# Performance work log

Hardware: AMD Instinct MI355X
Metric: run time of the kernel (lower is better)

The kernel has to match this reference:

```python
import jax, jax.numpy as jnp
import numpy as np

EPS = 1e-5  # BatchNorm eps
B, T, D, H, C = 64, 1024, 128, 1024, 128


def _glorot(k, shape):
    lim = float(np.sqrt(6.0 / (shape[0] + shape[1])))
    return jax.random.uniform(k, shape, minval=-lim, maxval=lim, dtype=jnp.float32)


def _bn(x, g, b, m, v):
    # eval-mode BatchNorm1d over the channel (last) dim
    return (x - m) * (g * jax.lax.rsqrt(v + EPS)) + b


def _cell(x, h, c, Wih, Whh, bias):
    # PyTorch LSTM gate order: i, f, g, o
    z = x @ Wih.T + h @ Whh.T + bias
    i, f, g, o = jnp.split(z, 4, axis=-1)
    c = jax.nn.sigmoid(f) * c + jax.nn.sigmoid(i) * jnp.tanh(g)
    h = jax.nn.sigmoid(o) * jnp.tanh(c)
    return h, c


def setup_inputs() -> dict:
    key = jax.random.key(0)
    ks = jax.random.split(key, 24)
    d = {}
    d['x'] = jax.random.normal(ks[0], (B, T, D), dtype=jnp.float32)
    # input BN (eval mode running stats + affine)
    d['ibn_g'] = jnp.ones((D,), jnp.float32); d['ibn_b'] = jnp.zeros((D,), jnp.float32)
    d['ibn_m'] = 0.1 * jax.random.normal(ks[1], (D,), jnp.float32)
    d['ibn_v'] = jnp.ones((D,), jnp.float32)
    # encoder LSTM (2 layers)
    d['enc_Wih0'] = _glorot(ks[2], (4 * H, D)); d['enc_Whh0'] = _glorot(ks[3], (4 * H, H))
    d['enc_b0'] = jnp.zeros((4 * H,), jnp.float32)
    d['enc_Wih1'] = _glorot(ks[4], (4 * H, H)); d['enc_Whh1'] = _glorot(ks[5], (4 * H, H))
    d['enc_b1'] = jnp.zeros((4 * H,), jnp.float32)
    # decoder LSTM (2 layers), layer0 input = num_classes
    d['dec_Wih0'] = _glorot(ks[6], (4 * H, C)); d['dec_Whh0'] = _glorot(ks[7], (4 * H, H))
    d['dec_b0'] = jnp.zeros((4 * H,), jnp.float32)
    d['dec_Wih1'] = _glorot(ks[8], (4 * H, H)); d['dec_Whh1'] = _glorot(ks[9], (4 * H, H))
    d['dec_b1'] = jnp.zeros((4 * H,), jnp.float32)
    # hidden BN
    d['hbn_g'] = jnp.ones((H,), jnp.float32); d['hbn_b'] = jnp.zeros((H,), jnp.float32)
    d['hbn_m'] = 0.1 * jax.random.normal(ks[10], (H,), jnp.float32)
    d['hbn_v'] = jnp.ones((H,), jnp.float32)
    # fc head: Linear(H,H) -> BN -> ReLU -> (Dropout=identity in eval) -> Linear(H,C)
    d['fc1_W'] = _glorot(ks[11], (H, H)); d['fc1_b'] = jnp.zeros((H,), jnp.float32)
    d['fbn_g'] = jnp.ones((H,), jnp.float32); d['fbn_b'] = jnp.zeros((H,), jnp.float32)
    d['fbn_m'] = 0.1 * jax.random.normal(ks[12], (H,), jnp.float32)
    d['fbn_v'] = jnp.ones((H,), jnp.float32)
    d['fc2_W'] = _glorot(ks[13], (C, H)); d['fc2_b'] = jnp.zeros((C,), jnp.float32)
    return d


def reference(x, ibn_g, ibn_b, ibn_m, ibn_v,
              enc_Wih0, enc_Whh0, enc_b0, enc_Wih1, enc_Whh1, enc_b1,
              dec_Wih0, dec_Whh0, dec_b0, dec_Wih1, dec_Whh1, dec_b1,
              hbn_g, hbn_b, hbn_m, hbn_v,
              fc1_W, fc1_b, fbn_g, fbn_b, fbn_m, fbn_v, fc2_W, fc2_b):
    b, t, _ = x.shape
    h = enc_Whh0.shape[1]
    c_dim = fc2_W.shape[0]
    xn = _bn(x, ibn_g, ibn_b, ibn_m, ibn_v)  # (B,T,D), per-channel BN

    def enc_step(carry, xt):
        h0, c0, h1, c1 = carry
        h0, c0 = _cell(xt, h0, c0, enc_Wih0, enc_Whh0, enc_b0)
        h1, c1 = _cell(h0, h1, c1, enc_Wih1, enc_Whh1, enc_b1)
        return (h0, c0, h1, c1), None

    z = jnp.zeros((b, h), x.dtype)
    (h0, c0, h1, c1), _ = jax.lax.scan(enc_step, (z, z, z, z), jnp.swapaxes(xn, 0, 1))

    def dec_step(carry, _):
        d0, e0, d1, e1, y = carry
        d0, e0 = _cell(y, d0, e0, dec_Wih0, dec_Whh0, dec_b0)
        d1, e1 = _cell(d0, d1, e1, dec_Wih1, dec_Whh1, dec_b1)
        hb = _bn(d1, hbn_g, hbn_b, hbn_m, hbn_v)
        f1 = jax.nn.relu(_bn(hb @ fc1_W.T + fc1_b, fbn_g, fbn_b, fbn_m, fbn_v))
        pred = f1 @ fc2_W.T + fc2_b  # (B, C)
        return (d0, e0, d1, e1, pred), pred

    y0 = jnp.zeros((b, c_dim), x.dtype)
    _, preds = jax.lax.scan(dec_step, (h0, c0, h1, c1, y0), None, length=t)
    return jnp.swapaxes(preds, 0, 1)  # (B, T, C)
```

## Files before the change

### kernel.cpp

```cpp
#include <hip/hip_runtime.h>
#include <hip/hip_bf16.h>


typedef __hip_bfloat16 hbf16;
typedef __bf16 bf16x8 __attribute__((ext_vector_type(8)));
typedef float f32x4 __attribute__((ext_vector_type(4)));
#define DEVI static __device__ __forceinline__

#define PITCH 2056
#define PITCH0 1160

DEVI float sigf(float x) { return 1.0f / (1.0f + __expf(-x)); }

DEVI bf16x8 as_bf(f32x4 v) { union { f32x4 f; bf16x8 b; } u; u.f = v; return u.b; }

DEVI void st_u32_coh(void* p, unsigned int v) {
  __hip_atomic_store((unsigned int*)p, v, __ATOMIC_RELAXED, __HIP_MEMORY_SCOPE_AGENT);
}
DEVI void st_u64_coh(void* p, unsigned long long v) {
  __hip_atomic_store((unsigned long long*)p, v, __ATOMIC_RELAXED, __HIP_MEMORY_SCOPE_AGENT);
}
DEVI void st_f32_coh(float* p, float v) {
  __hip_atomic_store(p, v, __ATOMIC_RELAXED, __HIP_MEMORY_SCOPE_AGENT);
}
DEVI unsigned short bf_bits(float v) {
  union { __hip_bfloat16 b; unsigned short s; } u;
  u.b = __float2bfloat16(v);
  return u.s;
}

DEVI void ld32_wait(f32x4* b, const hbf16* ap) {
  asm volatile(
    "global_load_dwordx4 %0, %32, off sc0 sc1\n\t"
    "global_load_dwordx4 %1, %32, off offset:64 sc0 sc1\n\t"
    "global_load_dwordx4 %2, %32, off offset:128 sc0 sc1\n\t"
    "global_load_dwordx4 %3, %32, off offset:192 sc0 sc1\n\t"
    "global_load_dwordx4 %4, %32, off offset:256 sc0 sc1\n\t"
    "global_load_dwordx4 %5, %32, off offset:320 sc0 sc1\n\t"
    "global_load_dwordx4 %6, %32, off offset:384 sc0 sc1\n\t"
    "global_load_dwordx4 %7, %32, off offset:448 sc0 sc1\n\t"
    "global_load_dwordx4 %8, %32, off offset:512 sc0 sc1\n\t"
    "global_load_dwordx4 %9, %32, off offset:576 sc0 sc1\n\t"
    "global_load_dwordx4 %10, %32, off offset:640 sc0 sc1\n\t"
    "global_load_dwordx4 %11, %32, off offset:704 sc0 sc1\n\t"
    "global_load_dwordx4 %12, %32, off offset:768 sc0 sc1\n\t"
    "global_load_dwordx4 %13, %32, off offset:832 sc0 sc1\n\t"
    "global_load_dwordx4 %14, %32, off offset:896 sc0 sc1\n\t"
    "global_load_dwordx4 %15, %32, off offset:960 sc0 sc1\n\t"
    "global_load_dwordx4 %16, %32, off offset:1024 sc0 sc1\n\t"
    "global_load_dwordx4 %17, %32, off offset:1088 sc0 sc1\n\t"
    "global_load_dwordx4 %18, %32, off offset:1152 sc0 sc1\n\t"
    "global_load_dwordx4 %19, %32, off offset:1216 sc0 sc1\n\t"
    "global_load_dwordx4 %20, %32, off offset:1280 sc0 sc1\n\t"
    "global_load_dwordx4 %21, %32, off offset:1344 sc0 sc1\n\t"
    "global_load_dwordx4 %22, %32, off offset:1408 sc0 sc1\n\t"
    "global_load_dwordx4 %23, %32, off offset:1472 sc0 sc1\n\t"
    "global_load_dwordx4 %24, %32, off offset:1536 sc0 sc1\n\t"
    "global_load_dwordx4 %25, %32, off offset:1600 sc0 sc1\n\t"
    "global_load_dwordx4 %26, %32, off offset:1664 sc0 sc1\n\t"
    "global_load_dwordx4 %27, %32, off offset:1728 sc0 sc1\n\t"
    "global_load_dwordx4 %28, %32, off offset:1792 sc0 sc1\n\t"
    "global_load_dwordx4 %29, %32, off offset:1856 sc0 sc1\n\t"
    "global_load_dwordx4 %30, %32, off offset:1920 sc0 sc1\n\t"
    "global_load_dwordx4 %31, %32, off offset:1984 sc0 sc1\n\t"
    "s_waitcnt vmcnt(0)"
    : "=&v"(b[0]), "=&v"(b[1]), "=&v"(b[2]), "=&v"(b[3]),
      "=&v"(b[4]), "=&v"(b[5]), "=&v"(b[6]), "=&v"(b[7]),
      "=&v"(b[8]), "=&v"(b[9]), "=&v"(b[10]), "=&v"(b[11]),
      "=&v"(b[12]), "=&v"(b[13]), "=&v"(b[14]), "=&v"(b[15]),
      "=&v"(b[16]), "=&v"(b[17]), "=&v"(b[18]), "=&v"(b[19]),
      "=&v"(b[20]), "=&v"(b[21]), "=&v"(b[22]), "=&v"(b[23]),
      "=&v"(b[24]), "=&v"(b[25]), "=&v"(b[26]), "=&v"(b[27]),
      "=&v"(b[28]), "=&v"(b[29]), "=&v"(b[30]), "=&v"(b[31])
    : "v"(ap) : "memory");
}

DEVI void ld4x8_wait(f32x4* b, const hbf16* a0, const hbf16* a1,
                     const hbf16* a2, const hbf16* a3) {
  asm volatile(
    "global_load_dwordx4 %0, %32, off sc0 sc1\n\t"
    "global_load_dwordx4 %1, %32, off offset:64 sc0 sc1\n\t"
    "global_load_dwordx4 %2, %32, off offset:128 sc0 sc1\n\t"
    "global_load_dwordx4 %3, %32, off offset:192 sc0 sc1\n\t"
    "global_load_dwordx4 %4, %32, off offset:256 sc0 sc1\n\t"
    "global_load_dwordx4 %5, %32, off offset:320 sc0 sc1\n\t"
    "global_load_dwordx4 %6, %32, off offset:384 sc0 sc1\n\t"
    "global_load_dwordx4 %7, %32, off offset:448 sc0 sc1\n\t"
    "global_load_dwordx4 %8, %33, off sc0 sc1\n\t"
    "global_load_dwordx4 %9, %33, off offset:64 sc0 sc1\n\t"
    "global_load_dwordx4 %10, %33, off offset:128 sc0 sc1\n\t"
    "global_load_dwordx4 %11, %33, off offset:192 sc0 sc1\n\t"
    "global_load_dwordx4 %12, %33, off offset:256 sc0 sc1\n\t"
    "global_load_dwordx4 %13, %33, off offset:320 sc0 sc1\n\t"
    "global_load_dwordx4 %14, %33, off offset:384 sc0 sc1\n\t"
    "global_load_dwordx4 %15, %33, off offset:448 sc0 sc1\n\t"
    "global_load_dwordx4 %16, %34, off sc0 sc1\n\t"
    "global_load_dwordx4 %17, %34, off offset:64 sc0 sc1\n\t"
    "global_load_dwordx4 %18, %34, off offset:128 sc0 sc1\n\t"
    "global_load_dwordx4 %19, %34, off offset:192 sc0 sc1\n\t"
    "global_load_dwordx4 %20, %34, off offset:256 sc0 sc1\n\t"
    "global_load_dwordx4 %21, %34, off offset:320 sc0 sc1\n\t"
    "global_load_dwordx4 %22, %34, off offset:384 sc0 sc1\n\t"
    "global_load_dwordx4 %23, %34, off offset:448 sc0 sc1\n\t"
    "global_load_dwordx4 %24, %35, off sc0 sc1\n\t"
    "global_load_dwordx4 %25, %35, off offset:64 sc0 sc1\n\t"
    "global_load_dwordx4 %26, %35, off offset:128 sc0 sc1\n\t"
    "global_load_dwordx4 %27, %35, off offset:192 sc0 sc1\n\t"
    "global_load_dwordx4 %28, %35, off offset:256 sc0 sc1\n\t"
    "global_load_dwordx4 %29, %35, off offset:320 sc0 sc1\n\t"
    "global_load_dwordx4 %30, %35, off offset:384 sc0 sc1\n\t"
    "global_load_dwordx4 %31, %35, off offset:448 sc0 sc1\n\t"
    "s_waitcnt vmcnt(0)"
    : "=&v"(b[0]), "=&v"(b[1]), "=&v"(b[2]), "=&v"(b[3]),
      "=&v"(b[4]), "=&v"(b[5]), "=&v"(b[6]), "=&v"(b[7]),
      "=&v"(b[8]), "=&v"(b[9]), "=&v"(b[10]), "=&v"(b[11]),
      "=&v"(b[12]), "=&v"(b[13]), "=&v"(b[14]), "=&v"(b[15]),
      "=&v"(b[16]), "=&v"(b[17]), "=&v"(b[18]), "=&v"(b[19]),
      "=&v"(b[20]), "=&v"(b[21]), "=&v"(b[22]), "=&v"(b[23]),
      "=&v"(b[24]), "=&v"(b[25]), "=&v"(b[26]), "=&v"(b[27]),
      "=&v"(b[28]), "=&v"(b[29]), "=&v"(b[30]), "=&v"(b[31])
    : "v"(a0), "v"(a1), "v"(a2), "v"(a3) : "memory");
}

DEVI void gbar(int* cnt8, int e) {
  asm volatile("s_waitcnt vmcnt(0) lgkmcnt(0)" ::: "memory");
  __syncthreads();
  if (threadIdx.x == 0)
    __hip_atomic_fetch_add(&cnt8[(blockIdx.x & 7) * 16], 1,
                           __ATOMIC_RELAXED, __HIP_MEMORY_SCOPE_AGENT);
  if (threadIdx.x < 8) {
    while (__hip_atomic_load(&cnt8[threadIdx.x * 16], __ATOMIC_RELAXED,
                             __HIP_MEMORY_SCOPE_AGENT) < e * 32)
      __builtin_amdgcn_s_sleep(1);
  }
  __syncthreads();
}

DEVI void fill_w(hbf16* W, int pitch, int koff, const hbf16* __restrict__ Wg,
                 int Kg, int base_h) {
  for (int r = (int)(threadIdx.x >> 3); r < 32; r += 32) {
    int g = r >> 3, hc = r & 7;
    const hbf16* src = Wg + (long)(g * 1024 + base_h + hc) * Kg;
    hbf16* dst = W + r * pitch + koff;
    for (int k = (threadIdx.x & 7) * 8; k < Kg; k += 64)
      *reinterpret_cast<bf16x8*>(dst + k) =
          *reinterpret_cast<const bf16x8*>(src + k);
  }
}

DEVI void seg_asm(f32x4& a0, f32x4& a1, const hbf16* __restrict__ A, long lda,
                  const hbf16* W, int pitch, int koff, int w, int q, int r16) {
  const hbf16* ap = A + (long)(w * 16 + r16) * lda + q * 8;
  const hbf16* w0 = W + r16 * pitch + koff + q * 8;
  const hbf16* w1 = W + (16 + r16) * pitch + koff + q * 8;
  f32x4 b[32];
  ld32_wait(b, ap);
#pragma unroll
  for (int k = 0; k < 32; ++k) {
    bf16x8 av = as_bf(b[k]);
    bf16x8 b0 = *reinterpret_cast<const bf16x8*>(w0 + k * 32);
    bf16x8 b1 = *reinterpret_cast<const bf16x8*>(w1 + k * 32);
    a0 = __builtin_amdgcn_mfma_f32_16x16x32_bf16(av, b0, a0, 0, 0, 0);
    a1 = __builtin_amdgcn_mfma_f32_16x16x32_bf16(av, b1, a1, 0, 0, 0);
  }
}

DEVI void seg_x(f32x4& a0, f32x4& a1, const hbf16* __restrict__ A, long lda,
                const hbf16* W, int pitch, int w, int q, int r16) {
  const hbf16* ap = A + (long)(w * 16 + r16) * lda + q * 8;
  const hbf16* w0 = W + r16 * pitch + q * 8;
  const hbf16* w1 = W + (16 + r16) * pitch + q * 8;
#pragma unroll
  for (int k = 0; k < 128; k += 32) {
    bf16x8 av = *reinterpret_cast<const bf16x8*>(ap + k);
    bf16x8 b0 = *reinterpret_cast<const bf16x8*>(w0 + k);
    bf16x8 b1 = *reinterpret_cast<const bf16x8*>(w1 + k);
    a0 = __builtin_amdgcn_mfma_f32_16x16x32_bf16(av, b0, a0, 0, 0, 0);
    a1 = __builtin_amdgcn_mfma_f32_16x16x32_bf16(av, b1, a1, 0, 0, 0);
  }
}

DEVI void mm4_asm(f32x4* pa, const hbf16* __restrict__ abase, const bf16x8* fr) {
  f32x4 b[32];
  ld4x8_wait(b, abase, abase + 16384, abase + 32768, abase + 49152);
#pragma unroll
  for (int i = 0; i < 8; ++i)
#pragma unroll
    for (int mt = 0; mt < 4; ++mt)
      pa[mt] = __builtin_amdgcn_mfma_f32_16x16x32_bf16(
          as_bf(b[mt * 8 + i]), fr[i], pa[mt], 0, 0, 0);
}

DEVI void cell(f32x4 a0, f32x4 a1, float bb0, float bb1, float* cst,
               hbf16* __restrict__ hout, int base_h, int lane, int w) {
  int q = lane >> 4, c = lane & 15;
#pragma unroll
  for (int r = 0; r < 4; ++r) {
    float z0 = a0[r] + bb0;
    float z1 = a1[r] + bb1;
    float zf = __shfl(z0, lane | 8, 64);
    float zo = __shfl(z1, lane | 8, 64);
    float hv = 0.f;
    if (c < 8) {
      float cn = sigf(zf) * cst[r] + sigf(z0) * tanhf(z1);
      cst[r] = cn;
      hv = sigf(zo) * tanhf(cn);
    }
    unsigned short my = bf_bits(hv);
    unsigned short nb = (unsigned short)__shfl((int)my, lane ^ 1, 64);
    if (c < 8 && (c & 1) == 0) {
      unsigned int pk = (unsigned int)my | ((unsigned int)nb << 16);
      st_u32_coh(hout + (long)(w * 16 + q * 4 + r) * 1024 + base_h + c, pk);
    }
  }
}

DEVI void store_c(const float* cst, float* cbuf, int hcol_g, int lane, int w) {
  int q = lane >> 4, c = lane & 15;
  if (c < 8) {
#pragma unroll
    for (int r = 0; r < 4; ++r)
      st_f32_coh(&cbuf[(long)(w * 16 + q * 4 + r) * 1024 + hcol_g], cst[r]);
  }
}

__global__ __launch_bounds__(256, 1) void k_enc(
    const hbf16* __restrict__ xb,
    const hbf16* __restrict__ Wih0f, const hbf16* __restrict__ Whh0,
    const hbf16* __restrict__ Wih1, const hbf16* __restrict__ Whh1,
    const float* __restrict__ b0f, const float* __restrict__ b1f,
    hbf16* h0_0, hbf16* h0_1, hbf16* h1_0, hbf16* h1_1,
    float* c0buf, float* c1buf, int* flags) {
  __shared__ hbf16 W[32 * PITCH];
  int wg = blockIdx.x, tid = threadIdx.x;
  int lane = tid & 63, w = tid >> 6, q = lane >> 4, c = lane & 15;
  bool isL0 = wg < 128;
  int cu = isL0 ? wg : wg - 128;
  int base_h = cu * 8;
  if (isL0) {
    fill_w(W, PITCH0, 0, Wih0f, 128, base_h);
    fill_w(W, PITCH0, 128, Whh0, 1024, base_h);
  } else {
    fill_w(W, PITCH, 0, Wih1, 1024, base_h);
    fill_w(W, PITCH, 1024, Whh1, 1024, base_h);
  }
  __syncthreads();
  const float* bias = isL0 ? b0f : b1f;
  float bb0 = bias[(c >> 3) * 1024 + base_h + (c & 7)];
  float bb1 = bias[(2 + (c >> 3)) * 1024 + base_h + (c & 7)];
  float cst[4] = {0.f, 0.f, 0.f, 0.f};
  int hcol_g = base_h + (c & 7);

  for (int t = 0; t <= 1024; ++t) {
    if (isL0) {
      if (t < 1024) {
        f32x4 a0 = {0.f,0.f,0.f,0.f}, a1 = {0.f,0.f,0.f,0.f};
        const hbf16* h0r = (t & 1) ? h0_0 : h0_1;
        seg_asm(a0, a1, h0r, 1024L, W, PITCH0, 128, w, q, c);
        seg_x(a0, a1, xb + (long)t * 128, 131072L, W, PITCH0, w, q, c);
        hbf16* h0w = (t & 1) ? h0_1 : h0_0;
        cell(a0, a1, bb0, bb1, cst, h0w, base_h, lane, w);
        if (t == 1023) store_c(cst, c0buf, hcol_g, lane, w);
      }
    } else {
      if (t >= 1) {
        f32x4 a0 = {0.f,0.f,0.f,0.f}, a1 = {0.f,0.f,0.f,0.f};
        const hbf16* h0r = (t & 1) ? h0_0 : h0_1;
        seg_asm(a0, a1, h0r, 1024L, W, PITCH, 0, w, q, c);
        const hbf16* h1r = (t & 1) ? h1_1 : h1_0;
        seg_asm(a0, a1, h1r, 1024L, W, PITCH, 1024, w, q, c);
        hbf16* h1w = (t & 1) ? h1_0 : h1_1;
        cell(a0, a1, bb0, bb1, cst, h1w, base_h, lane, w);
        if (t == 1024) store_c(cst, c1buf, hcol_g, lane, w);
      }
    }
    if (t < 1024) gbar(flags, t + 1);
  }
}

__global__ __launch_bounds__(256, 1) void k_dec(
    const hbf16* __restrict__ Wfold, const hbf16* __restrict__ Whh0d,
    const hbf16* __restrict__ Wih1d, const hbf16* __restrict__ Whh1d,
    const float* __restrict__ b0t, const float* __restrict__ b0p,
    const float* __restrict__ b1d,
    const hbf16* __restrict__ fc1Wf, const float* __restrict__ fc1bf,
    const float* __restrict__ fs2, const float* __restrict__ fadd2,
    const hbf16* __restrict__ fc2Wb, const float* __restrict__ fc2b,
    hbf16* d0_0, hbf16* d0_1, hbf16* d1_0, hbf16* d1_1, hbf16* f1b,
    const float* __restrict__ c0buf, const float* __restrict__ c1buf,
    float* __restrict__ out, int* flags) {
  __shared__ hbf16 W[32 * PITCH];
  __shared__ float bounce[4][64][16];
  int wg = blockIdx.x, tid = threadIdx.x;
  int lane = tid & 63, w = tid >> 6, q = lane >> 4, c = lane & 15;
  bool isP1 = wg < 128;
  int cu = isP1 ? wg : wg - 128;
  int base_h = cu * 8;
  if (isP1) {
    fill_w(W, PITCH, 0, Wfold, 1024, base_h);
    fill_w(W, PITCH, 1024, Whh0d, 1024, base_h);
  } else {
    fill_w(W, PITCH, 0, Wih1d, 1024, base_h);
    fill_w(W, PITCH, 1024, Whh1d, 1024, base_h);
  }
  __syncthreads();
  int gi0 = (c >> 3) * 1024 + base_h + (c & 7);
  int gi1 = (2 + (c >> 3)) * 1024 + base_h + (c & 7);
  float bt0, bt1, bp0, bp1;
  if (isP1) { bt0 = b0t[gi0]; bt1 = b0t[gi1]; bp0 = b0p[gi0]; bp1 = b0p[gi1]; }
  else      { bt0 = b1d[gi0]; bt1 = b1d[gi1]; bp0 = bt0;      bp1 = bt1; }
  int hcol_g = base_h + (c & 7);
  float cst[4] = {0.f, 0.f, 0.f, 0.f};
  {
    const float* cb = isP1 ? c0buf : c1buf;
    if (c < 8) {
#pragma unroll
      for (int r = 0; r < 4; ++r)
        cst[r] = cb[(long)(w * 16 + q * 4 + r) * 1024 + hcol_g];
    }
  }
  bool isP3 = (wg < 64);
  bool isPred = (wg >= 128 && wg < 136);
  bf16x8 fr[8];
#pragma unroll
  for (int i = 0; i < 8; ++i) fr[i] = bf16x8{0,0,0,0,0,0,0,0};
  float e_b[4] = {0,0,0,0}, e_s[4] = {0,0,0,0}, e_a[4] = {0,0,0,0};
  int red_row = tid >> 2, red_c4 = (tid & 3) * 4;
  if (isP3) {
    const hbf16* fp = fc1Wf + (long)(wg * 16 + c) * 1024 + w * 256 + q * 8;
#pragma unroll
    for (int i = 0; i < 8; ++i) fr[i] = *reinterpret_cast<const bf16x8*>(fp + i * 32);
#pragma unroll
    for (int i = 0; i < 4; ++i) {
      int col = wg * 16 + red_c4 + i;
      e_b[i] = fc1bf[col]; e_s[i] = fs2[col]; e_a[i] = fadd2[col];
    }
  } else if (isPred) {
    const hbf16* fp = fc2Wb + (long)((wg - 128) * 16 + c) * 1024 + w * 256 + q * 8;
#pragma unroll
    for (int i = 0; i < 8; ++i) fr[i] = *reinterpret_cast<const bf16x8*>(fp + i * 32);
#pragma unroll
    for (int i = 0; i < 4; ++i) e_b[i] = fc2b[(wg - 128) * 16 + red_c4 + i];
  }

  f32x4 r0 = {0.f,0.f,0.f,0.f}, r1 = {0.f,0.f,0.f,0.f};

  for (int t = 0; t <= 1024; ++t) {
    if (isP1 && t < 1024) {
      f32x4 a0 = r0, a1 = r1;
      if (t > 0) {
        seg_asm(a0, a1, f1b, 1024L, W, PITCH, 0, w, q, c);
      } else {
        seg_asm(a0, a1, d0_1, 1024L, W, PITCH, 1024, w, q, c);
      }
      float B0 = (t > 0) ? bt0 : bp0, B1 = (t > 0) ? bt1 : bp1;
      hbf16* d0w = (t & 1) ? d0_1 : d0_0;
      cell(a0, a1, B0, B1, cst, d0w, base_h, lane, w);
    }
    if (!isP1 && t == 0) {
      seg_asm(r0, r1, d1_1, 1024L, W, PITCH, 1024, w, q, c);
    }
    if (isPred && t >= 1) {
      f32x4 pa[4] = {{0.f,0.f,0.f,0.f},{0.f,0.f,0.f,0.f},{0.f,0.f,0.f,0.f},{0.f,0.f,0.f,0.f}};
      mm4_asm(pa, f1b + (long)c * 1024 + w * 256 + q * 8, fr);
#pragma unroll
      for (int mt = 0; mt < 4; ++mt)
#pragma unroll
        for (int r = 0; r < 4; ++r) bounce[w][mt * 16 + q * 4 + r][c] = pa[mt][r];
      __syncthreads();
#pragma unroll
      for (int i = 0; i < 4; ++i) {
        int cc = red_c4 + i;
        float s = bounce[0][red_row][cc] + bounce[1][red_row][cc] +
                  bounce[2][red_row][cc] + bounce[3][red_row][cc] + e_b[i];
        out[(long)red_row * 131072 + (long)(t - 1) * 128 + (wg - 128) * 16 + cc] = s;
      }
    }
    if (t == 1024) break;
    gbar(flags, 3 * t + 1);
    if (!isP1) {
      f32x4 a0 = r0, a1 = r1;
      const hbf16* d0c = (t & 1) ? d0_1 : d0_0;
      seg_asm(a0, a1, d0c, 1024L, W, PITCH, 0, w, q, c);
      hbf16* d1w = (t & 1) ? d1_1 : d1_0;
      cell(a0, a1, bt0, bt1, cst, d1w, base_h, lane, w);
    } else if (isP3 && t < 1023) {
      r0 = f32x4{0.f,0.f,0.f,0.f}; r1 = f32x4{0.f,0.f,0.f,0.f};
      const hbf16* d0n = (t & 1) ? d0_1 : d0_0;
      seg_asm(r0, r1, d0n, 1024L, W, PITCH, 1024, w, q, c);
    }
    gbar(flags, 3 * t + 2);
    if (isP3) {
      const hbf16* d1c = (t & 1) ? d1_1 : d1_0;
      f32x4 pa[4] = {{0.f,0.f,0.f,0.f},{0.f,0.f,0.f,0.f},{0.f,0.f,0.f,0.f},{0.f,0.f,0.f,0.f}};
      mm4_asm(pa, d1c + (long)c * 1024 + w * 256 + q * 8, fr);
#pragma unroll
      for (int mt = 0; mt < 4; ++mt)
#pragma unroll
        for (int r = 0; r < 4; ++r) bounce[w][mt * 16 + q * 4 + r][c] = pa[mt][r];
      __syncthreads();
#pragma unroll
      for (int i = 0; i < 4; ++i) {
        int cc = red_c4 + i;
        float s = bounce[0][red_row][cc] + bounce[1][red_row][cc] +
                  bounce[2][red_row][cc] + bounce[3][red_row][cc];
        float v = fmaxf((s + e_b[i]) * e_s[i] + e_a[i], 0.f);
        bounce[0][red_row][cc] = v;
      }
      {
        union { unsigned short s4[4]; unsigned long long u; } pk;
#pragma unroll
        for (int i = 0; i < 4; ++i) pk.s4[i] = bf_bits(bounce[0][red_row][red_c4 + i]);
        st_u64_coh(f1b + (long)red_row * 1024 + wg * 16 + red_c4, pk.u);
      }
    } else if (isP1 && t < 1023) {
      r0 = f32x4{0.f,0.f,0.f,0.f}; r1 = f32x4{0.f,0.f,0.f,0.f};
      const hbf16* d0n = (t & 1) ? d0_1 : d0_0;
      seg_asm(r0, r1, d0n, 1024L, W, PITCH, 1024, w, q, c);
    }
    if (!isP1 && t < 1023) {
      r0 = f32x4{0.f,0.f,0.f,0.f}; r1 = f32x4{0.f,0.f,0.f,0.f};
      const hbf16* d1n = (t & 1) ? d1_1 : d1_0;
      seg_asm(r0, r1, d1n, 1024L, W, PITCH, 1024, w, q, c);
    }
    gbar(flags, 3 * t + 3);
  }
}


__global__ void k_cast_bf16(const float* __restrict__ s, hbf16* __restrict__ d, long n) {
  long i = (long)blockIdx.x * blockDim.x + threadIdx.x;
  long stride = (long)gridDim.x * blockDim.x;
  for (; i < n; i += stride) d[i] = __float2bfloat16(s[i]);
}

__global__ void k_prep_b0tot(const float* __restrict__ dec_b0, const float* __restrict__ dWih0,
                             const float* __restrict__ fc2b, float* __restrict__ b0d_tot) {
  int n = blockIdx.x * 256 + threadIdx.x;
  float acc = 0.f;
  for (int cc = 0; cc < 128; ++cc) acc += dWih0[n * 128 + cc] * fc2b[cc];
  b0d_tot[n] = dec_b0[n] + acc;
}

__global__ void k_fold_ih0(const float* __restrict__ g, const float* __restrict__ bb,
                           const float* __restrict__ m, const float* __restrict__ v,
                           const float* __restrict__ Wm, const float* __restrict__ b0,
                           hbf16* __restrict__ Wf, float* __restrict__ biasf) {
  int n = blockIdx.x * 256 + threadIdx.x;
  float acc = 0.f;
  for (int k = 0; k < 128; ++k) {
    float s = g[k] * rsqrtf(v[k] + 1e-5f);
    float tt = bb[k] - m[k] * s;
    float wv = Wm[n * 128 + k];
    Wf[n * 128 + k] = __float2bfloat16(wv * s);
    acc += tt * wv;
  }
  biasf[n] = b0[n] + acc;
}

__global__ void k_fold_fc1(const float* __restrict__ hg, const float* __restrict__ hb,
                           const float* __restrict__ hm, const float* __restrict__ hv,
                           const float* __restrict__ Wm, const float* __restrict__ fb,
                           const float* __restrict__ fg, const float* __restrict__ fbb,
                           const float* __restrict__ fm, const float* __restrict__ fv,
                           hbf16* __restrict__ Wf, float* __restrict__ bfo,
                           float* __restrict__ fs2, float* __restrict__ fadd2) {
  int n = blockIdx.x * 256 + threadIdx.x;
  float acc = 0.f;
  for (int k = 0; k < 1024; ++k) {
    float s = hg[k] * rsqrtf(hv[k] + 1e-5f);
    float tt = hb[k] - hm[k] * s;
    float wv = Wm[(long)n * 1024 + k];
    Wf[(long)n * 1024 + k] = __float2bfloat16(wv * s);
    acc += tt * wv;
  }
  bfo[n] = fb[n] + acc;
  float s2 = fg[n] * rsqrtf(fv[n] + 1e-5f);
  fs2[n] = s2;
  fadd2[n] = fbb[n] - fm[n] * s2;
}

__global__ void k_fold_wf(const float* __restrict__ Wih0d, const float* __restrict__ fc2W,
                          hbf16* __restrict__ Wfold) {
  long gid = (long)blockIdx.x * 256 + threadIdx.x;
  int n = (int)(gid >> 10), jcol = (int)(gid & 1023);
  float acc = 0.f;
  for (int cc = 0; cc < 128; ++cc)
    acc += Wih0d[n * 128 + cc] * fc2W[cc * 1024 + jcol];
  Wfold[gid] = __float2bfloat16(acc);
}


extern "C" void kernel_launch(void* const* d_in, const int* in_sizes, int n_in,
                              void* d_out, int out_size, void* d_ws, size_t ws_size,
                              hipStream_t stream) {
  (void)in_sizes; (void)n_in; (void)out_size; (void)ws_size;
  const float* x     = (const float*)d_in[0];
  const float* ibn_g = (const float*)d_in[1];
  const float* ibn_b = (const float*)d_in[2];
  const float* ibn_m = (const float*)d_in[3];
  const float* ibn_v = (const float*)d_in[4];
  const float* eWih0 = (const float*)d_in[5];
  const float* eWhh0 = (const float*)d_in[6];
  const float* e_b0  = (const float*)d_in[7];
  const float* eWih1 = (const float*)d_in[8];
  const float* eWhh1 = (const float*)d_in[9];
  const float* e_b1  = (const float*)d_in[10];
  const float* dWih0 = (const float*)d_in[11];
  const float* dWhh0 = (const float*)d_in[12];
  const float* d_b0  = (const float*)d_in[13];
  const float* dWih1 = (const float*)d_in[14];
  const float* dWhh1 = (const float*)d_in[15];
  const float* d_b1  = (const float*)d_in[16];
  const float* hbn_g = (const float*)d_in[17];
  const float* hbn_b = (const float*)d_in[18];
  const float* hbn_m = (const float*)d_in[19];
  const float* hbn_v = (const float*)d_in[20];
  const float* fc1_W = (const float*)d_in[21];
  const float* fc1_b = (const float*)d_in[22];
  const float* fbn_g = (const float*)d_in[23];
  const float* fbn_b = (const float*)d_in[24];
  const float* fbn_m = (const float*)d_in[25];
  const float* fbn_v = (const float*)d_in[26];
  const float* fc2_W = (const float*)d_in[27];
  const float* fc2_b = (const float*)d_in[28];
  float* out = (float*)d_out;

  char* p = (char*)d_ws;
  auto alloc = [&](size_t bytes) -> void* {
    void* r = (void*)p;
    p += (bytes + 255) & ~(size_t)255;
    return r;
  };
  hbf16* xb     = (hbf16*)alloc(64L * 1024 * 128 * 2);
  hbf16* Wih0f  = (hbf16*)alloc(4096L * 128 * 2);
  hbf16* Whh0e  = (hbf16*)alloc(4096L * 1024 * 2);
  hbf16* Wih1e  = (hbf16*)alloc(4096L * 1024 * 2);
  hbf16* Whh1e  = (hbf16*)alloc(4096L * 1024 * 2);
  hbf16* Wfold  = (hbf16*)alloc(4096L * 1024 * 2);
  hbf16* Whh0d  = (hbf16*)alloc(4096L * 1024 * 2);
  hbf16* Wih1d  = (hbf16*)alloc(4096L * 1024 * 2);
  hbf16* Whh1d  = (hbf16*)alloc(4096L * 1024 * 2);
  hbf16* fc1Wf  = (hbf16*)alloc(1024L * 1024 * 2);
  hbf16* fc2Wb  = (hbf16*)alloc(128L * 1024 * 2);
  float* bias0f = (float*)alloc(4096 * 4);
  float* b0dtot = (float*)alloc(4096 * 4);
  float* fc1bf  = (float*)alloc(1024 * 4);
  float* fs2    = (float*)alloc(1024 * 4);
  float* fadd2  = (float*)alloc(1024 * 4);
  char* st = p;
  hbf16* h0_0 = (hbf16*)alloc(64L * 1024 * 2);
  hbf16* h0_1 = (hbf16*)alloc(64L * 1024 * 2);
  hbf16* h1_0 = (hbf16*)alloc(64L * 1024 * 2);
  hbf16* h1_1 = (hbf16*)alloc(64L * 1024 * 2);
  float* c0b  = (float*)alloc(64L * 1024 * 4);
  float* c1b  = (float*)alloc(64L * 1024 * 4);
  hbf16* f1b  = (hbf16*)alloc(64L * 1024 * 2);
  int*   flagsE = (int*)alloc(256 * 4);
  int*   flagsD = (int*)alloc(256 * 4);
  size_t stbytes = (size_t)(p - st);

  hipMemsetAsync(st, 0, stbytes, stream);

  k_cast_bf16<<<4096, 256, 0, stream>>>(x, xb, 64L * 1024 * 128);
  k_cast_bf16<<<2048, 256, 0, stream>>>(eWhh0, Whh0e, 4096L * 1024);
  k_cast_bf16<<<2048, 256, 0, stream>>>(eWih1, Wih1e, 4096L * 1024);
  k_cast_bf16<<<2048, 256, 0, stream>>>(eWhh1, Whh1e, 4096L * 1024);
  k_cast_bf16<<<2048, 256, 0, stream>>>(dWhh0, Whh0d, 4096L * 1024);
  k_cast_bf16<<<2048, 256, 0, stream>>>(dWih1, Wih1d, 4096L * 1024);
  k_cast_bf16<<<2048, 256, 0, stream>>>(dWhh1, Whh1d, 4096L * 1024);
  k_cast_bf16<<<512, 256, 0, stream>>>(fc2_W, fc2Wb, 128L * 1024);
  k_prep_b0tot<<<16, 256, 0, stream>>>(d_b0, dWih0, fc2_b, b0dtot);
  k_fold_ih0<<<16, 256, 0, stream>>>(ibn_g, ibn_b, ibn_m, ibn_v, eWih0, e_b0, Wih0f, bias0f);
  k_fold_fc1<<<4, 256, 0, stream>>>(hbn_g, hbn_b, hbn_m, hbn_v, fc1_W, fc1_b,
                                    fbn_g, fbn_b, fbn_m, fbn_v, fc1Wf, fc1bf, fs2, fadd2);
  k_fold_wf<<<16384, 256, 0, stream>>>(dWih0, fc2_W, Wfold);

  k_enc<<<256, 256, 0, stream>>>(xb, Wih0f, Whh0e, Wih1e, Whh1e, bias0f, e_b1,
                                 h0_0, h0_1, h1_0, h1_1, c0b, c1b, flagsE);

  k_dec<<<256, 256, 0, stream>>>(Wfold, Whh0d, Wih1d, Whh1d, b0dtot, d_b0, d_b1,
                                 fc1Wf, fc1bf, fs2, fadd2, fc2Wb, fc2_b,
                                 h0_0, h0_1, h1_0, h1_1, f1b, c0b, c1b, out, flagsD);
}
```

Baseline: 39.17 ms.

## Use per-timestep ring buffers for hidden states to allow plain cached loads

Measured after the change: 39.69 ms. About the same (+1.3%).

```diff
diff --git a/kernel.cpp b/kernel.cpp
--- a/kernel.cpp
+++ b/kernel.cpp
@@ -9,6 +9,8 @@
 
 #define PITCH 2056
 #define PITCH0 1160
+#define SLE 66048L
+#define SLDATA 65536L
 
 DEVI float sigf(float x) { return 1.0f / (1.0f + __expf(-x)); }
 
@@ -165,6 +167,21 @@
   }
 }
 
+DEVI void seg_pl(f32x4& a0, f32x4& a1, const hbf16* A,
+                 const hbf16* W, int pitch, int koff, int w, int q, int r16) {
+  const hbf16* ap = A + (long)(w * 16 + r16) * 1024L + q * 8;
+  const hbf16* w0 = W + r16 * pitch + koff + q * 8;
+  const hbf16* w1 = W + (16 + r16) * pitch + koff + q * 8;
+#pragma unroll
+  for (int k = 0; k < 32; ++k) {
+    bf16x8 av = *reinterpret_cast<const bf16x8*>(ap + k * 32);
+    bf16x8 b0 = *reinterpret_cast<const bf16x8*>(w0 + k * 32);
+    bf16x8 b1 = *reinterpret_cast<const bf16x8*>(w1 + k * 32);
+    a0 = __builtin_amdgcn_mfma_f32_16x16x32_bf16(av, b0, a0, 0, 0, 0);
+    a1 = __builtin_amdgcn_mfma_f32_16x16x32_bf16(av, b1, a1, 0, 0, 0);
+  }
+}
+
 DEVI void seg_x(f32x4& a0, f32x4& a1, const hbf16* __restrict__ A, long lda,
                 const hbf16* W, int pitch, int w, int q, int r16) {
   const hbf16* ap = A + (long)(w * 16 + r16) * lda + q * 8;
@@ -191,8 +208,24 @@
           as_bf(b[mt * 8 + i]), fr[i], pa[mt], 0, 0, 0);
 }
 
+DEVI void mm4_pl(f32x4* pa, const hbf16* abase, const bf16x8* fr) {
+  f32x4 b[32];
+#pragma unroll
+  for (int mt = 0; mt < 4; ++mt)
+#pragma unroll
+    for (int i = 0; i < 8; ++i)
+      b[mt * 8 + i] = *reinterpret_cast<const f32x4*>(
+          reinterpret_cast<const char*>(abase + mt * 16384) + i * 64);
+#pragma unroll
+  for (int i = 0; i < 8; ++i)
+#pragma unroll
+    for (int mt = 0; mt < 4; ++mt)
+      pa[mt] = __builtin_amdgcn_mfma_f32_16x16x32_bf16(
+          as_bf(b[mt * 8 + i]), fr[i], pa[mt], 0, 0, 0);
+}
+
 DEVI void cell(f32x4 a0, f32x4 a1, float bb0, float bb1, float* cst,
-               hbf16* __restrict__ hout, int base_h, int lane, int w) {
+               hbf16* hout, int base_h, int lane, int w) {
   int q = lane >> 4, c = lane & 15;
 #pragma unroll
   for (int r = 0; r < 4; ++r) {
@@ -224,12 +257,14 @@
   }
 }
 
+template<int RING>
 __global__ __launch_bounds__(256, 1) void k_enc(
     const hbf16* __restrict__ xb,
     const hbf16* __restrict__ Wih0f, const hbf16* __restrict__ Whh0,
     const hbf16* __restrict__ Wih1, const hbf16* __restrict__ Whh1,
     const float* __restrict__ b0f, const float* __restrict__ b1f,
     hbf16* h0_0, hbf16* h0_1, hbf16* h1_0, hbf16* h1_1,
+    hbf16* rh0, hbf16* rh1,
     float* c0buf, float* c1buf, int* flags) {
   __shared__ hbf16 W[32 * PITCH];
   int wg = blockIdx.x, tid = threadIdx.x;
@@ -255,22 +290,34 @@
     if (isL0) {
       if (t < 1024) {
         f32x4 a0 = {0.f,0.f,0.f,0.f}, a1 = {0.f,0.f,0.f,0.f};
-        const hbf16* h0r = (t & 1) ? h0_0 : h0_1;
-        seg_asm(a0, a1, h0r, 1024L, W, PITCH0, 128, w, q, c);
-        seg_x(a0, a1, xb + (long)t * 128, 131072L, W, PITCH0, w, q, c);
-        hbf16* h0w = (t & 1) ? h0_1 : h0_0;
-        cell(a0, a1, bb0, bb1, cst, h0w, base_h, lane, w);
+        if constexpr (RING) {
+          seg_pl(a0, a1, rh0 + (long)t * SLE, W, PITCH0, 128, w, q, c);
+          seg_x(a0, a1, xb + (long)t * 128, 131072L, W, PITCH0, w, q, c);
+          cell(a0, a1, bb0, bb1, cst, rh0 + (long)(t + 1) * SLE, base_h, lane, w);
+        } else {
+          const hbf16* h0r = (t & 1) ? h0_0 : h0_1;
+          seg_asm(a0, a1, h0r, 1024L, W, PITCH0, 128, w, q, c);
+          seg_x(a0, a1, xb + (long)t * 128, 131072L, W, PITCH0, w, q, c);
+          hbf16* h0w = (t & 1) ? h0_1 : h0_0;
+          cell(a0, a1, bb0, bb1, cst, h0w, base_h, lane, w);
+        }
         if (t == 1023) store_c(cst, c0buf, hcol_g, lane, w);
       }
     } else {
       if (t >= 1) {
         f32x4 a0 = {0.f,0.f,0.f,0.f}, a1 = {0.f,0.f,0.f,0.f};
-        const hbf16* h0r = (t & 1) ? h0_0 : h0_1;
-        seg_asm(a0, a1, h0r, 1024L, W, PITCH, 0, w, q, c);
-        const hbf16* h1r = (t & 1) ? h1_1 : h1_0;
-        seg_asm(a0, a1, h1r, 1024L, W, PITCH, 1024, w, q, c);
-        hbf16* h1w = (t & 1) ? h1_0 : h1_1;
-        cell(a0, a1, bb0, bb1, cst, h1w, base_h, lane, w);
+        if constexpr (RING) {
+          seg_pl(a0, a1, rh0 + (long)t * SLE, W, PITCH, 0, w, q, c);
+          seg_pl(a0, a1, rh1 + (long)(t - 1) * SLE, W, PITCH, 1024, w, q, c);
+          cell(a0, a1, bb0, bb1, cst, rh1 + (long)t * SLE, base_h, lane, w);
+        } else {
+          const hbf16* h0r = (t & 1) ? h0_0 : h0_1;
+          seg_asm(a0, a1, h0r, 1024L, W, PITCH, 0, w, q, c);
+          const hbf16* h1r = (t & 1) ? h1_1 : h1_0;
+          seg_asm(a0, a1, h1r, 1024L, W, PITCH, 1024, w, q, c);
+          hbf16* h1w = (t & 1) ? h1_0 : h1_1;
+          cell(a0, a1, bb0, bb1, cst, h1w, base_h, lane, w);
+        }
         if (t == 1024) store_c(cst, c1buf, hcol_g, lane, w);
       }
     }
@@ -278,6 +325,7 @@
   }
 }
 
+template<int RING>
 __global__ __launch_bounds__(256, 1) void k_dec(
     const hbf16* __restrict__ Wfold, const hbf16* __restrict__ Whh0d,
     const hbf16* __restrict__ Wih1d, const hbf16* __restrict__ Whh1d,
@@ -287,6 +335,8 @@
     const float* __restrict__ fs2, const float* __restrict__ fadd2,
     const hbf16* __restrict__ fc2Wb, const float* __restrict__ fc2b,
     hbf16* d0_0, hbf16* d0_1, hbf16* d1_0, hbf16* d1_1, hbf16* f1b,
+    hbf16* rf1, hbf16* rd0, hbf16* rd1,
+    const hbf16* h0fin, const hbf16* h1fin,
     const float* __restrict__ c0buf, const float* __restrict__ c1buf,
     float* __restrict__ out, int* flags) {
   __shared__ hbf16 W[32 * PITCH];
@@ -349,20 +399,32 @@
     if (isP1 && t < 1024) {
       f32x4 a0 = r0, a1 = r1;
       if (t > 0) {
-        seg_asm(a0, a1, f1b, 1024L, W, PITCH, 0, w, q, c);
+        if constexpr (RING)
+          seg_pl(a0, a1, rf1 + (long)(t - 1) * SLE, W, PITCH, 0, w, q, c);
+        else
+          seg_asm(a0, a1, f1b, 1024L, W, PITCH, 0, w, q, c);
       } else {
-        seg_asm(a0, a1, d0_1, 1024L, W, PITCH, 1024, w, q, c);
+        if constexpr (RING)
+          seg_pl(a0, a1, h0fin, W, PITCH, 1024, w, q, c);
+        else
+          seg_asm(a0, a1, d0_1, 1024L, W, PITCH, 1024, w, q, c);
       }
       float B0 = (t > 0) ? bt0 : bp0, B1 = (t > 0) ? bt1 : bp1;
-      hbf16* d0w = (t & 1) ? d0_1 : d0_0;
+      hbf16* d0w = RING ? (rd0 + (long)t * SLE) : ((t & 1) ? d0_1 : d0_0);
       cell(a0, a1, B0, B1, cst, d0w, base_h, lane, w);
     }
     if (!isP1 && t == 0) {
-      seg_asm(r0, r1, d1_1, 1024L, W, PITCH, 1024, w, q, c);
+      if constexpr (RING)
+        seg_pl(r0, r1, h1fin, W, PITCH, 1024, w, q, c);
+      else
+        seg_asm(r0, r1, d1_1, 1024L, W, PITCH, 1024, w, q, c);
     }
     if (isPred && t >= 1) {
       f32x4 pa[4] = {{0.f,0.f,0.f,0.f},{0.f,0.f,0.f,0.f},{0.f,0.f,0.f,0.f},{0.f,0.f,0.f,0.f}};
-      mm4_asm(pa, f1b + (long)c * 1024 + w * 256 + q * 8, fr);
+      if constexpr (RING)
+        mm4_pl(pa, rf1 + (long)(t - 1) * SLE + (long)c * 1024 + w * 256 + q * 8, fr);
+      else
+        mm4_asm(pa, f1b + (long)c * 1024 + w * 256 + q * 8, fr);
 #pragma unroll
       for (int mt = 0; mt < 4; ++mt)
 #pragma unroll
@@ -380,20 +442,33 @@
     gbar(flags, 3 * t + 1);
     if (!isP1) {
       f32x4 a0 = r0, a1 = r1;
-      const hbf16* d0c = (t & 1) ? d0_1 : d0_0;
-      seg_asm(a0, a1, d0c, 1024L, W, PITCH, 0, w, q, c);
-      hbf16* d1w = (t & 1) ? d1_1 : d1_0;
-      cell(a0, a1, bt0, bt1, cst, d1w, base_h, lane, w);
+      if constexpr (RING) {
+        seg_pl(a0, a1, rd0 + (long)t * SLE, W, PITCH, 0, w, q, c);
+        cell(a0, a1, bt0, bt1, cst, rd1 + (long)t * SLE, base_h, lane, w);
+      } else {
+        const hbf16* d0c = (t & 1) ? d0_1 : d0_0;
+        seg_asm(a0, a1, d0c, 1024L, W, PITCH, 0, w, q, c);
+        hbf16* d1w = (t & 1) ? d1_1 : d1_0;
+        cell(a0, a1, bt0, bt1, cst, d1w, base_h, lane, w);
+      }
     } else if (isP3 && t < 1023) {
       r0 = f32x4{0.f,0.f,0.f,0.f}; r1 = f32x4{0.f,0.f,0.f,0.f};
-      const hbf16* d0n = (t & 1) ? d0_1 : d0_0;
-      seg_asm(r0, r1, d0n, 1024L, W, PITCH, 1024, w, q, c);
+      if constexpr (RING)
+        seg_pl(r0, r1, rd0 + (long)t * SLE, W, PITCH, 1024, w, q, c);
+      else {
+        const hbf16* d0n = (t & 1) ? d0_1 : d0_0;
+        seg_asm(r0, r1, d0n, 1024L, W, PITCH, 1024, w, q, c);
+      }
     }
     gbar(flags, 3 * t + 2);
     if (isP3) {
-      const hbf16* d1c = (t & 1) ? d1_1 : d1_0;
       f32x4 pa[4] = {{0.f,0.f,0.f,0.f},{0.f,0.f,0.f,0.f},{0.f,0.f,0.f,0.f},{0.f,0.f,0.f,0.f}};
-      mm4_asm(pa, d1c + (long)c * 1024 + w * 256 + q * 8, fr);
+      if constexpr (RING)
+        mm4_pl(pa, rd1 + (long)t * SLE + (long)c * 1024 + w * 256 + q * 8, fr);
+      else {
+        const hbf16* d1c = (t & 1) ? d1_1 : d1_0;
+        mm4_asm(pa, d1c + (long)c * 1024 + w * 256 + q * 8, fr);
+      }
 #pragma unroll
       for (int mt = 0; mt < 4; ++mt)
 #pragma unroll
@@ -411,17 +486,26 @@
         union { unsigned short s4[4]; unsigned long long u; } pk;
 #pragma unroll
         for (int i = 0; i < 4; ++i) pk.s4[i] = bf_bits(bounce[0][red_row][red_c4 + i]);
-        st_u64_coh(f1b + (long)red_row * 1024 + wg * 16 + red_c4, pk.u);
+        hbf16* f1dst = RING ? (rf1 + (long)t * SLE) : f1b;
+        st_u64_coh(f1dst + (long)red_row * 1024 + wg * 16 + red_c4, pk.u);
       }
     } else if (isP1 && t < 1023) {
       r0 = f32x4{0.f,0.f,0.f,0.f}; r1 = f32x4{0.f,0.f,0.f,0.f};
-      const hbf16* d0n = (t & 1) ? d0_1 : d0_0;
-      seg_asm(r0, r1, d0n, 1024L, W, PITCH, 1024, w, q, c);
+      if constexpr (RING)
+        seg_pl(r0, r1, rd0 + (long)t * SLE, W, PITCH, 1024, w, q, c);
+      else {
+        const hbf16* d0n = (t & 1) ? d0_1 : d0_0;
+        seg_asm(r0, r1, d0n, 1024L, W, PITCH, 1024, w, q, c);
+      }
     }
     if (!isP1 && t < 1023) {
       r0 = f32x4{0.f,0.f,0.f,0.f}; r1 = f32x4{0.f,0.f,0.f,0.f};
-      const hbf16* d1n = (t & 1) ? d1_1 : d1_0;
-      seg_asm(r0, r1, d1n, 1024L, W, PITCH, 1024, w, q, c);
+      if constexpr (RING)
+        seg_pl(r0, r1, rd1 + (long)t * SLE, W, PITCH, 1024, w, q, c);
+      else {
+        const hbf16* d1n = (t & 1) ? d1_1 : d1_0;
+        seg_asm(r0, r1, d1n, 1024L, W, PITCH, 1024, w, q, c);
+      }
     }
     gbar(flags, 3 * t + 3);
   }
@@ -494,7 +578,7 @@
 extern "C" void kernel_launch(void* const* d_in, const int* in_sizes, int n_in,
                               void* d_out, int out_size, void* d_ws, size_t ws_size,
                               hipStream_t stream) {
-  (void)in_sizes; (void)n_in; (void)out_size; (void)ws_size;
+  (void)in_sizes; (void)n_in; (void)out_size;
   const float* x     = (const float*)d_in[0];
   const float* ibn_g = (const float*)d_in[1];
   const float* ibn_b = (const float*)d_in[2];
@@ -560,7 +644,19 @@
   int*   flagsD = (int*)alloc(256 * 4);
   size_t stbytes = (size_t)(p - st);
 
+  hbf16* rh0 = (hbf16*)alloc(1025L * SLE * 2);
+  hbf16* rh1 = (hbf16*)alloc(1025L * SLE * 2);
+  hbf16* rf1 = (hbf16*)alloc(1024L * SLE * 2);
+  hbf16* rd0 = (hbf16*)alloc(1024L * SLE * 2);
+  hbf16* rd1 = (hbf16*)alloc(1024L * SLE * 2);
+  size_t need = (size_t)(p - (char*)d_ws);
+  bool use_ring = (ws_size >= need);
+
   hipMemsetAsync(st, 0, stbytes, stream);
+  if (use_ring) {
+    hipMemsetAsync(rh0, 0, SLDATA * 2, stream);
+    hipMemsetAsync(rh1, 0, SLDATA * 2, stream);
+  }
 
   k_cast_bf16<<<4096, 256, 0, stream>>>(x, xb, 64L * 1024 * 128);
   k_cast_bf16<<<2048, 256, 0, stream>>>(eWhh0, Whh0e, 4096L * 1024);
@@ -576,10 +672,25 @@
                                     fbn_g, fbn_b, fbn_m, fbn_v, fc1Wf, fc1bf, fs2, fadd2);
   k_fold_wf<<<16384, 256, 0, stream>>>(dWih0, fc2_W, Wfold);
 
-  k_enc<<<256, 256, 0, stream>>>(xb, Wih0f, Whh0e, Wih1e, Whh1e, bias0f, e_b1,
-                                 h0_0, h0_1, h1_0, h1_1, c0b, c1b, flagsE);
-
-  k_dec<<<256, 256, 0, stream>>>(Wfold, Whh0d, Wih1d, Whh1d, b0dtot, d_b0, d_b1,
-                                 fc1Wf, fc1bf, fs2, fadd2, fc2Wb, fc2_b,
-                                 h0_0, h0_1, h1_0, h1_1, f1b, c0b, c1b, out, flagsD);
-}
+  if (use_ring) {
+    k_enc<1><<<256, 256, 0, stream>>>(xb, Wih0f, Whh0e, Wih1e, Whh1e, bias0f, e_b1,
+                                      h0_0, h0_1, h1_0, h1_1, rh0, rh1,
+                                      c0b, c1b, flagsE);
+    k_dec<1><<<256, 256, 0, stream>>>(Wfold, Whh0d, Wih1d, Whh1d, b0dtot, d_b0, d_b1,
+                                      fc1Wf, fc1bf, fs2, fadd2, fc2Wb, fc2_b,
+                                      h0_0, h0_1, h1_0, h1_1, f1b,
+                                      rf1, rd0, rd1,
+                                      rh0 + 1024L * SLE, rh1 + 1024L * SLE,
+                                      c0b, c1b, out, flagsD);
+  } else {
+    k_enc<0><<<256, 256, 0, stream>>>(xb, Wih0f, Whh0e, Wih1e, Whh1e, bias0f, e_b1,
+                                      h0_0, h0_1, h1_0, h1_1, rh0, rh1,
+                                      c0b, c1b, flagsE);
+    k_dec<0><<<256, 256, 0, stream>>>(Wfold, Whh0d, Wih1d, Whh1d, b0dtot, d_b0, d_b1,
+                                      fc1Wf, fc1bf, fs2, fadd2, fc2Wb, fc2_b,
+                                      h0_0, h0_1, h1_0, h1_1, f1b,
+                                      rf1, rd0, rd1,
+                                      h0_1, h1_1,
+                                      c0b, c1b, out, flagsD);
+  }
+}
```
